# Kernel optimization log

Measured on AMD Instinct MI355X. Metric: run time of the kernel, lower is better.

Reference implementation:

```python
import jax, jax.numpy as jnp
import numpy as np

LAMBDA_COOR = 5.0
LAMBDA_NOOBJ = 0.5


def setup_inputs() -> dict:
    key = jax.random.key(0)
    k1, k2 = jax.random.split(key)
    B, W, H, C = 128, 256, 256, 5
    outputs = jax.random.normal(k1, (B, W, H, C), dtype=jnp.float32)
    targets = jax.random.normal(k2, (B, W, H, C), dtype=jnp.float32)
    return {"outputs": outputs, "targets": targets}


def reference(outputs, targets):
    # channel layout per cell: (conf, x, y, w, h)
    conf_pred = outputs[..., 0]
    conf_gt = targets[..., 0]
    obj_mask = conf_gt > 0
    # sum of squared coord errors (x, y, w, h) per cell: [B, W, H]
    coord_sq = jnp.sum((outputs[..., 1:] - targets[..., 1:]) ** 2, axis=-1)
    obj_loss = LAMBDA_COOR * coord_sq + (conf_pred - 1.0) ** 2
    noobj_loss = LAMBDA_NOOBJ * conf_pred ** 2
    loss = jnp.sum(jnp.where(obj_mask, obj_loss, noobj_loss))
    return loss / outputs.shape[0]
```

## Files before the change

### kernel.cpp

```cpp
#include <hip/hip_runtime.h>

#define LAMBDA_COOR 5.0f
#define LAMBDA_NOOBJ 0.5f

constexpr int TPB = 256;
constexpr int WAVES_PER_BLOCK = TPB / 64;
constexpr int WAVE_F4 = 5 * 64;
constexpr int WAVE_FLOATS = WAVE_F4 * 4;

__global__ __launch_bounds__(TPB) void yolo_loss_kernel(
    const float4* __restrict__ outp4, const float4* __restrict__ tgt4,
    float* __restrict__ loss, int n_wtiles, float inv_b)
{
    __shared__ float so[WAVES_PER_BLOCK][WAVE_FLOATS];
    __shared__ float st[WAVES_PER_BLOCK][WAVE_FLOATS];

    const int lane  = threadIdx.x & 63;
    const int wid   = threadIdx.x >> 6;
    const int gwave = blockIdx.x * WAVES_PER_BLOCK + wid;
    const int nwaves = gridDim.x * WAVES_PER_BLOCK;

    float acc = 0.0f;

    for (int w = gwave; w < n_wtiles; w += nwaves) {
        const size_t base4 = (size_t)w * WAVE_F4;

        float4 vo[5], vt[5];
        #pragma unroll
        for (int k = 0; k < 5; ++k) {
            vo[k] = outp4[base4 + (size_t)(k * 64 + lane)];
            vt[k] = tgt4 [base4 + (size_t)(k * 64 + lane)];
        }

        float4* so4 = (float4*)so[wid];
        float4* st4 = (float4*)st[wid];
        #pragma unroll
        for (int k = 0; k < 5; ++k) {
            so4[k * 64 + lane] = vo[k];
            st4[k * 64 + lane] = vt[k];
        }

        const float* o = &so[wid][20 * lane];
        const float* t = &st[wid][20 * lane];
        #pragma unroll
        for (int c = 0; c < 4; ++c) {
            const float* oc = o + 5 * c;
            const float* tc = t + 5 * c;
            float conf = oc[0];
            float coord = 0.0f;
            #pragma unroll
            for (int k = 1; k < 5; ++k) {
                float d = oc[k] - tc[k];
                coord = fmaf(d, d, coord);
            }
            float obj   = fmaf(LAMBDA_COOR, coord, (conf - 1.0f) * (conf - 1.0f));
            float noobj = LAMBDA_NOOBJ * conf * conf;
            acc += (tc[0] > 0.0f) ? obj : noobj;
        }
    }

    #pragma unroll
    for (int off = 32; off > 0; off >>= 1)
        acc += __shfl_down(acc, off, 64);

    __shared__ float wave_sums[WAVES_PER_BLOCK];
    if (lane == 0) wave_sums[wid] = acc;
    __syncthreads();

    if (threadIdx.x == 0) {
        float s = 0.0f;
        #pragma unroll
        for (int i = 0; i < WAVES_PER_BLOCK; ++i) s += wave_sums[i];
        atomicAdd(loss, s * inv_b);
    }
}

extern "C" void kernel_launch(void* const* d_in, const int* in_sizes, int n_in,
                              void* d_out, int out_size, void* d_ws, size_t ws_size,
                              hipStream_t stream) {
    const float4* outputs = (const float4*)d_in[0];
    const float4* targets = (const float4*)d_in[1];
    float* loss = (float*)d_out;

    const int n_elems  = in_sizes[0];
    const int n_wtiles = n_elems / WAVE_FLOATS;
    const float inv_b  = 1.0f / 128.0f;

    hipMemsetAsync(d_out, 0, sizeof(float), stream);

    const int blocks = 2048;
    yolo_loss_kernel<<<blocks, TPB, 0, stream>>>(
        outputs, targets, loss, n_wtiles, inv_b);
}
```

Baseline: 335.2 us.

## Replace LDS-staged grid-stride loop with direct per-thread nontemporal vector loads

Each thread now loads its own 20 contiguous floats (5 float4) per group straight into registers with nontemporal loads, so the LDS transpose staging is gone. The kernel launches one thread per two groups and drops the grid-stride loop, so all loads are issued up front. Per-thread strided 80-byte accesses are less coalesced across the wave than the old layout. The grid size assumes the element count divides evenly, with no tail handling.

```diff
diff --git a/kernel.cpp b/kernel.cpp
--- a/kernel.cpp
+++ b/kernel.cpp
@@ -4,44 +4,42 @@
 #define LAMBDA_NOOBJ 0.5f
 
 constexpr int TPB = 256;
-constexpr int WAVES_PER_BLOCK = TPB / 64;
-constexpr int WAVE_F4 = 5 * 64;
-constexpr int WAVE_FLOATS = WAVE_F4 * 4;
+constexpr int GROUPS_PER_THREAD = 2;
+
+typedef float v4f __attribute__((ext_vector_type(4)));
 
 __global__ __launch_bounds__(TPB) void yolo_loss_kernel(
-    const float4* __restrict__ outp4, const float4* __restrict__ tgt4,
-    float* __restrict__ loss, int n_wtiles, float inv_b)
+    const v4f* __restrict__ o4, const v4f* __restrict__ t4,
+    float* __restrict__ loss, float inv_b)
 {
-    __shared__ float so[WAVES_PER_BLOCK][WAVE_FLOATS];
-    __shared__ float st[WAVES_PER_BLOCK][WAVE_FLOATS];
+    const int tid = blockIdx.x * TPB + threadIdx.x;
+    const int nthreads = gridDim.x * TPB;
 
-    const int lane  = threadIdx.x & 63;
-    const int wid   = threadIdx.x >> 6;
-    const int gwave = blockIdx.x * WAVES_PER_BLOCK + wid;
-    const int nwaves = gridDim.x * WAVES_PER_BLOCK;
+    v4f vo[GROUPS_PER_THREAD][5], vt[GROUPS_PER_THREAD][5];
+    #pragma unroll
+    for (int b = 0; b < GROUPS_PER_THREAD; ++b) {
+        const size_t g = (size_t)tid + (size_t)b * nthreads;
+        const v4f* ob = o4 + g * 5;
+        const v4f* tb = t4 + g * 5;
+        #pragma unroll
+        for (int k = 0; k < 5; ++k) {
+            vo[b][k] = __builtin_nontemporal_load(ob + k);
+            vt[b][k] = __builtin_nontemporal_load(tb + k);
+        }
+    }
 
     float acc = 0.0f;
-
-    for (int w = gwave; w < n_wtiles; w += nwaves) {
-        const size_t base4 = (size_t)w * WAVE_F4;
-
-        float4 vo[5], vt[5];
+    #pragma unroll
+    for (int b = 0; b < GROUPS_PER_THREAD; ++b) {
+        float o[20], t[20];
         #pragma unroll
         for (int k = 0; k < 5; ++k) {
-            vo[k] = outp4[base4 + (size_t)(k * 64 + lane)];
-            vt[k] = tgt4 [base4 + (size_t)(k * 64 + lane)];
+            #pragma unroll
+            for (int j = 0; j < 4; ++j) {
+                o[4 * k + j] = vo[b][k][j];
+                t[4 * k + j] = vt[b][k][j];
+            }
         }
-
-        float4* so4 = (float4*)so[wid];
-        float4* st4 = (float4*)st[wid];
-        #pragma unroll
-        for (int k = 0; k < 5; ++k) {
-            so4[k * 64 + lane] = vo[k];
-            st4[k * 64 + lane] = vt[k];
-        }
-
-        const float* o = &so[wid][20 * lane];
-        const float* t = &st[wid][20 * lane];
         #pragma unroll
         for (int c = 0; c < 4; ++c) {
             const float* oc = o + 5 * c;
@@ -63,14 +61,16 @@
     for (int off = 32; off > 0; off >>= 1)
         acc += __shfl_down(acc, off, 64);
 
-    __shared__ float wave_sums[WAVES_PER_BLOCK];
+    __shared__ float wave_sums[TPB / 64];
+    const int lane = threadIdx.x & 63;
+    const int wid  = threadIdx.x >> 6;
     if (lane == 0) wave_sums[wid] = acc;
     __syncthreads();
 
     if (threadIdx.x == 0) {
         float s = 0.0f;
         #pragma unroll
-        for (int i = 0; i < WAVES_PER_BLOCK; ++i) s += wave_sums[i];
+        for (int i = 0; i < TPB / 64; ++i) s += wave_sums[i];
         atomicAdd(loss, s * inv_b);
     }
 }
@@ -78,17 +78,17 @@
 extern "C" void kernel_launch(void* const* d_in, const int* in_sizes, int n_in,
                               void* d_out, int out_size, void* d_ws, size_t ws_size,
                               hipStream_t stream) {
-    const float4* outputs = (const float4*)d_in[0];
-    const float4* targets = (const float4*)d_in[1];
+    const v4f* outputs = (const v4f*)d_in[0];
+    const v4f* targets = (const v4f*)d_in[1];
     float* loss = (float*)d_out;
 
     const int n_elems  = in_sizes[0];
-    const int n_wtiles = n_elems / WAVE_FLOATS;
-    const float inv_b  = 1.0f / 128.0f;
+    const int n_groups = n_elems / 20;
+    const int threads_total = n_groups / GROUPS_PER_THREAD;
+    const int blocks = threads_total / TPB;
+    const float inv_b = 1.0f / 128.0f;
 
     hipMemsetAsync(d_out, 0, sizeof(float), stream);
 
-    const int blocks = 2048;
-    yolo_loss_kernel<<<blocks, TPB, 0, stream>>>(
-        outputs, targets, loss, n_wtiles, inv_b);
+    yolo_loss_kernel<<<blocks, TPB, 0, stream>>>(outputs, targets, loss, inv_b);
 }
```

Result: slower. 370.2 us (+10.4%).
